# Kernel tuning notes

Hardware: AMD Instinct MI355X
Metric: run time of the kernel (lower is better)

## Reference

```python
import jax, jax.numpy as jnp
import numpy as np

S, D, P, R, E, M, K = 1024, 1024, 2816, 64, 8, 16, 1


def setup_inputs() -> dict:
    key = jax.random.key(0)
    ks = jax.random.split(key, 10)
    xav_a = (2.0 / (P + R)) ** 0.5   # xavier_uniform-like std for adapters
    xav_d = (2.0 / (D + P)) ** 0.5   # xavier for down projections
    bank_s = (1.0 / D) ** 0.5        # keep basis columns O(1)
    return {
        "hidden_states": jax.random.normal(ks[0], (S, D), jnp.float32),
        "expert_indices": jax.random.randint(ks[1], (S, K), 0, E),
        "expert_weights": jax.random.uniform(ks[2], (S, K), jnp.float32),
        "up_adapters": jax.random.normal(ks[3], (E, P, R), jnp.float32) * xav_a,
        "gate_adapters": jax.random.normal(ks[4], (E, P, R), jnp.float32) * xav_a,
        "up_mixture_logits": jax.random.normal(ks[5], (E, M), jnp.float32) * 0.01,
        "gate_mixture_logits": jax.random.normal(ks[6], (E, M), jnp.float32) * 0.01,
        "down_projections": jax.random.normal(ks[7], (E, D, P), jnp.float32) * xav_d,
        "up_bank": jax.random.normal(ks[8], (M, D, R), jnp.float32) * bank_s,
        "gate_bank": jax.random.normal(ks[9], (M, D, R), jnp.float32) * bank_s,
    }


def reference(hidden_states, expert_indices, expert_weights,
              up_adapters, gate_adapters, up_mixture_logits,
              gate_mixture_logits, down_projections, up_bank, gate_bank):
    n_experts = down_projections.shape[0]
    # SparseMixer: token-independent mixture weights over global bases (softmax)
    alpha_up = jax.nn.softmax(up_mixture_logits, axis=-1)      # [E, M]
    alpha_gate = jax.nn.softmax(gate_mixture_logits, axis=-1)  # [E, M]
    # Compose per-expert mixed bases: sum_j alpha_{e,j} B_j -> [E, D, R]
    up_mixed = jnp.einsum('em,mdr->edr', alpha_up, up_bank)
    gate_mixed = jnp.einsum('em,mdr->edr', alpha_gate, gate_bank)
    # Recomposed Up/Gate weights: A_e @ mixed_e^T -> [E, P, D]
    W_up = jnp.einsum('epr,edr->epd', up_adapters, up_mixed)
    W_gate = jnp.einsum('epr,edr->epd', gate_adapters, gate_mixed)
    # Combine routing weights per (token, expert): sum over topk slots
    onehot = (expert_indices[..., None] == jnp.arange(n_experts)).astype(hidden_states.dtype)  # [S,K,E]
    comb = jnp.einsum('ske,sk->se', onehot, expert_weights)  # [S, E]
    out = jnp.zeros_like(hidden_states)
    for e in range(n_experts):  # fixed small expert count
        up = hidden_states @ W_up[e].T        # [S, P]
        gate = hidden_states @ W_gate[e].T    # [S, P]
        inter = jax.nn.silu(gate) * up        # gated activation
        out = out + (inter @ down_projections[e].T) * comb[:, e:e + 1]
    return out
```

## Files before the change

kernel.cpp:

```cpp
#include <hip/hip_runtime.h>
#include <hip/hip_bf16.h>
#include <math.h>

#define S 1024
#define D 1024
#define P 2816
#define R 64
#define E 8
#define M 16
#define DSPLIT 4
#define KSPLIT 2
#define KHALF (P / KSPLIT)

typedef __attribute__((ext_vector_type(8))) short short8;
typedef __attribute__((ext_vector_type(4))) float floatx4;

static __device__ inline unsigned short f2bf(float f) {
  __hip_bfloat16 h = __float2bfloat16(f);
  return *reinterpret_cast<unsigned short*>(&h);
}

__global__ __launch_bounds__(256) void k_zero(float* __restrict__ out) {
  int i = blockIdx.x * 256 + threadIdx.x;
  *(float4*)(out + (size_t)i * 4) = make_float4(0.f, 0.f, 0.f, 0.f);
}

__global__ __launch_bounds__(256) void k_mix(
    const float* __restrict__ up_logits, const float* __restrict__ gate_logits,
    const float* __restrict__ up_bank, const float* __restrict__ gate_bank,
    unsigned short* __restrict__ mxu, unsigned short* __restrict__ mxg) {
  __shared__ float alpha[2][E][M];
  int t = threadIdx.x;
  if (t < 16) {
    int mat = t >> 3, e = t & 7;
    const float* lg = (mat ? gate_logits : up_logits) + e * M;
    float v[M], mx = -1e30f, s = 0.f;
#pragma unroll
    for (int m = 0; m < M; ++m) { v[m] = lg[m]; mx = fmaxf(mx, v[m]); }
#pragma unroll
    for (int m = 0; m < M; ++m) { v[m] = expf(v[m] - mx); s += v[m]; }
#pragma unroll
    for (int m = 0; m < M; ++m) alpha[mat][e][m] = v[m] / s;
  }
  __syncthreads();
  int g = blockIdx.x * 256 + t;
  int d = g >> 6, r = g & 63;
  float au[E] = {0, 0, 0, 0, 0, 0, 0, 0}, ag[E] = {0, 0, 0, 0, 0, 0, 0, 0};
#pragma unroll
  for (int m = 0; m < M; ++m) {
    float vu = up_bank[((size_t)m * D + d) * R + r];
    float vg = gate_bank[((size_t)m * D + d) * R + r];
#pragma unroll
    for (int e = 0; e < E; ++e) {
      au[e] += alpha[0][e][m] * vu;
      ag[e] += alpha[1][e][m] * vg;
    }
  }
#pragma unroll
  for (int e = 0; e < E; ++e) {
    mxu[((size_t)e * D + d) * R + r] = f2bf(au[e]);
    mxg[((size_t)e * D + d) * R + r] = f2bf(ag[e]);
  }
}

__global__ __launch_bounds__(1024) void k_sort(
    const int* __restrict__ idx, int* __restrict__ perm, int* __restrict__ offs) {
  __shared__ int hist[E];
  __shared__ int base[E];
  int t = threadIdx.x;
  if (t < E) hist[t] = 0;
  __syncthreads();
  int e = idx[t];
  atomicAdd(&hist[e], 1);
  __syncthreads();
  if (t == 0) {
    int run = 0;
    for (int i = 0; i < E; ++i) { base[i] = run; offs[i] = run; run += hist[i]; }
    offs[E] = S;
  }
  __syncthreads();
  int pos = atomicAdd(&base[e], 1);
  perm[pos] = t;
}

__global__ __launch_bounds__(256) void k_t(
    const float* __restrict__ H, const unsigned short* __restrict__ mxu,
    const unsigned short* __restrict__ mxg, const int* __restrict__ perm,
    const int* __restrict__ offs, float* __restrict__ tpart) {
  int e = blockIdx.x;
  int start = offs[e] + blockIdx.y * 128;
  int end = offs[e + 1];
  if (start >= end) return;
  int z = blockIdx.z;
  __shared__ unsigned short As[128][72];
  __shared__ unsigned short Bs[128][72];
  int t = threadIdx.x;
  int lane = t & 63, w = t >> 6, quad = lane >> 4, l15 = lane & 15;
  floatx4 acc[2][8];
#pragma unroll
  for (int tt = 0; tt < 2; ++tt)
#pragma unroll
    for (int nt = 0; nt < 8; ++nt) acc[tt][nt] = (floatx4){0.f, 0.f, 0.f, 0.f};

  int row_cache[4];
#pragma unroll
  for (int j = 0; j < 4; ++j) {
    int c = t + j * 256;
    int arow = c >> 3;
    int pos = start + arow;
    row_cache[j] = (pos < end) ? perm[pos] : -1;
  }

  for (int it = 0; it < 4; ++it) {
    int k0 = z * 256 + it * 64;
#pragma unroll
    for (int j = 0; j < 4; ++j) {
      int c = t + j * 256;
      int arow = c >> 3, acol = (c & 7) * 8;
      short8 v = (short8){0, 0, 0, 0, 0, 0, 0, 0};
      if (row_cache[j] >= 0) {
        const float* src = H + (size_t)row_cache[j] * D + k0 + acol;
        float4 f0 = *(const float4*)src;
        float4 f1 = *(const float4*)(src + 4);
        v[0] = f2bf(f0.x); v[1] = f2bf(f0.y); v[2] = f2bf(f0.z); v[3] = f2bf(f0.w);
        v[4] = f2bf(f1.x); v[5] = f2bf(f1.y); v[6] = f2bf(f1.z); v[7] = f2bf(f1.w);
      }
      *(short8*)&As[arow][acol] = v;
    }
    {
      int dd = t >> 2, r0 = (t & 3) * 16;
      const unsigned short* su = mxu + ((size_t)e * D + k0 + dd) * R + r0;
      const unsigned short* sg = mxg + ((size_t)e * D + k0 + dd) * R + r0;
      short8 u0 = *(const short8*)su, u1 = *(const short8*)(su + 8);
      short8 g0 = *(const short8*)sg, g1 = *(const short8*)(sg + 8);
#pragma unroll
      for (int j = 0; j < 8; ++j) {
        Bs[r0 + j][dd] = u0[j];
        Bs[r0 + 8 + j][dd] = u1[j];
        Bs[64 + r0 + j][dd] = g0[j];
        Bs[64 + r0 + 8 + j][dd] = g1[j];
      }
    }
    __syncthreads();
#pragma unroll
    for (int ks = 0; ks < 2; ++ks) {
      int kc = ks * 32 + quad * 8;
      short8 a[2], b[8];
#pragma unroll
      for (int tt = 0; tt < 2; ++tt) a[tt] = *(const short8*)&As[w * 32 + tt * 16 + l15][kc];
#pragma unroll
      for (int nt = 0; nt < 8; ++nt) b[nt] = *(const short8*)&Bs[nt * 16 + l15][kc];
#pragma unroll
      for (int tt = 0; tt < 2; ++tt)
#pragma unroll
        for (int nt = 0; nt < 8; ++nt)
          acc[tt][nt] = __builtin_amdgcn_mfma_f32_16x16x32_bf16(a[tt], b[nt], acc[tt][nt], 0, 0, 0);
    }
    __syncthreads();
  }
#pragma unroll
  for (int tt = 0; tt < 2; ++tt)
#pragma unroll
    for (int reg = 0; reg < 4; ++reg) {
      int row = w * 32 + tt * 16 + quad * 4 + reg;
      int pos = start + row;
      if (pos < end) {
#pragma unroll
        for (int nt = 0; nt < 8; ++nt)
          tpart[((size_t)z * S + pos) * 128 + nt * 16 + l15] = acc[tt][nt][reg];
      }
    }
}

__global__ __launch_bounds__(256) void k_tred(
    const float* __restrict__ tpart, unsigned short* __restrict__ tbuf) {
  int i = blockIdx.x * 256 + threadIdx.x;
  float s = 0.f;
#pragma unroll
  for (int ds = 0; ds < DSPLIT; ++ds) s += tpart[(size_t)ds * S * 128 + i];
  tbuf[i] = f2bf(s);
}

__global__ __launch_bounds__(256) void k_inter(
    const unsigned short* __restrict__ tbuf, const float* __restrict__ Aup,
    const float* __restrict__ Agate, const int* __restrict__ offs,
    unsigned short* __restrict__ inter) {
  int e = blockIdx.x;
  int start = offs[e] + blockIdx.y * 64;
  int end = offs[e + 1];
  if (start >= end) return;
  int p0 = blockIdx.z * 128;
  __shared__ unsigned short Ts[64][136];
  __shared__ unsigned short Bu[128][72];
  __shared__ unsigned short Bg[128][72];
  int t = threadIdx.x;
  int lane = t & 63, w = t >> 6;
#pragma unroll
  for (int j = 0; j < 4; ++j) {
    int i = t + j * 256;
    int row = i >> 4, c8 = (i & 15) * 8;
    int pos = start + row;
    float4 v = (pos < end) ? *(const float4*)(tbuf + (size_t)pos * 128 + c8)
                           : make_float4(0.f, 0.f, 0.f, 0.f);
    *(float4*)&Ts[row][c8] = v;
  }
#pragma unroll
  for (int j = 0; j < 4; ++j) {
    int i = t + j * 256;
    int pr = i >> 3, c8 = (i & 7) * 8;
    const float* su = Aup + ((size_t)(e * P + p0 + pr) * R + c8);
    const float* sg = Agate + ((size_t)(e * P + p0 + pr) * R + c8);
    float4 u0 = *(const float4*)su, u1 = *(const float4*)(su + 4);
    float4 g0 = *(const float4*)sg, g1 = *(const float4*)(sg + 4);
    short8 uv, gv;
    uv[0] = f2bf(u0.x); uv[1] = f2bf(u0.y); uv[2] = f2bf(u0.z); uv[3] = f2bf(u0.w);
    uv[4] = f2bf(u1.x); uv[5] = f2bf(u1.y); uv[6] = f2bf(u1.z); uv[7] = f2bf(u1.w);
    gv[0] = f2bf(g0.x); gv[1] = f2bf(g0.y); gv[2] = f2bf(g0.z); gv[3] = f2bf(g0.w);
    gv[4] = f2bf(g1.x); gv[5] = f2bf(g1.y); gv[6] = f2bf(g1.z); gv[7] = f2bf(g1.w);
    *(short8*)&Bu[pr][c8] = uv;
    *(short8*)&Bg[pr][c8] = gv;
  }
  __syncthreads();
  int quad = lane >> 4, l15 = lane & 15;
  floatx4 au_acc[4][2], ag_acc[4][2];
#pragma unroll
  for (int tt = 0; tt < 4; ++tt)
#pragma unroll
    for (int pt = 0; pt < 2; ++pt) {
      au_acc[tt][pt] = (floatx4){0.f, 0.f, 0.f, 0.f};
      ag_acc[tt][pt] = (floatx4){0.f, 0.f, 0.f, 0.f};
    }
#pragma unroll
  for (int ks = 0; ks < 2; ++ks) {
    int kc = ks * 32 + quad * 8;
    short8 au[4], ag[4], bu[2], bg[2];
#pragma unroll
    for (int tt = 0; tt < 4; ++tt) {
      au[tt] = *(const short8*)&Ts[tt * 16 + l15][kc];
      ag[tt] = *(const short8*)&Ts[tt * 16 + l15][64 + kc];
    }
#pragma unroll
    for (int pt = 0; pt < 2; ++pt) {
      bu[pt] = *(const short8*)&Bu[w * 32 + pt * 16 + l15][kc];
      bg[pt] = *(const short8*)&Bg[w * 32 + pt * 16 + l15][kc];
    }
#pragma unroll
    for (int tt = 0; tt < 4; ++tt)
#pragma unroll
      for (int pt = 0; pt < 2; ++pt) {
        au_acc[tt][pt] = __builtin_amdgcn_mfma_f32_16x16x32_bf16(au[tt], bu[pt], au_acc[tt][pt], 0, 0, 0);
        ag_acc[tt][pt] = __builtin_amdgcn_mfma_f32_16x16x32_bf16(ag[tt], bg[pt], ag_acc[tt][pt], 0, 0, 0);
      }
  }
#pragma unroll
  for (int tt = 0; tt < 4; ++tt)
#pragma unroll
    for (int reg = 0; reg < 4; ++reg) {
      int row = tt * 16 + quad * 4 + reg;
      int pos = start + row;
      if (pos < end) {
#pragma unroll
        for (int pt = 0; pt < 2; ++pt) {
          float g = ag_acc[tt][pt][reg];
          float u = au_acc[tt][pt][reg];
          float val = u * (g / (1.f + __expf(-g)));
          inter[(size_t)pos * P + p0 + w * 32 + pt * 16 + l15] = f2bf(val);
        }
      }
    }
}

__global__ __launch_bounds__(256) void k_down(
    const unsigned short* __restrict__ inter, const float* __restrict__ Wd,
    const int* __restrict__ perm, const int* __restrict__ offs,
    const float* __restrict__ wts, float* __restrict__ out) {
  int e = blockIdx.x;
  int start = offs[e];
  int end = offs[e + 1];
  if (start >= end) return;
  int kz = blockIdx.y;
  int d0 = blockIdx.z * 32;
  __shared__ unsigned short As[256][72];
  __shared__ unsigned short Bs[32][72];
  int t = threadIdx.x;
  int lane = t & 63, w = t >> 6, quad = lane >> 4, l15 = lane & 15;
  int brow = t >> 3, bcol = (t & 7) * 8;
  const float* bsrc = Wd + ((size_t)(e * D + d0 + brow) * P + bcol + kz * KHALF);
  floatx4 acc[4][2];
#pragma unroll
  for (int tt = 0; tt < 4; ++tt)
#pragma unroll
    for (int dt = 0; dt < 2; ++dt) acc[tt][dt] = (floatx4){0.f, 0.f, 0.f, 0.f};

  for (int it = 0; it < KHALF / 64; ++it) {
    int k0 = kz * KHALF + it * 64;
    {
      float4 b0 = *(const float4*)(bsrc + it * 64);
      float4 b1 = *(const float4*)(bsrc + it * 64 + 4);
      short8 bv;
      bv[0] = f2bf(b0.x); bv[1] = f2bf(b0.y); bv[2] = f2bf(b0.z); bv[3] = f2bf(b0.w);
      bv[4] = f2bf(b1.x); bv[5] = f2bf(b1.y); bv[6] = f2bf(b1.z); bv[7] = f2bf(b1.w);
      *(short8*)&Bs[brow][bcol] = bv;
    }
#pragma unroll
    for (int j = 0; j < 8; ++j) {
      int c = t + j * 256;
      int arow = c >> 3, acol = (c & 7) * 8;
      int pos = start + arow;
      float4 v = (pos < end) ? *(const float4*)(inter + (size_t)pos * P + k0 + acol)
                             : make_float4(0.f, 0.f, 0.f, 0.f);
      *(float4*)&As[arow][acol] = v;
    }
    __syncthreads();
#pragma unroll
    for (int ks = 0; ks < 2; ++ks) {
      int kc = ks * 32 + quad * 8;
      short8 a[4], b[2];
#pragma unroll
      for (int tt = 0; tt < 4; ++tt) a[tt] = *(const short8*)&As[w * 64 + tt * 16 + l15][kc];
#pragma unroll
      for (int dt = 0; dt < 2; ++dt) b[dt] = *(const short8*)&Bs[dt * 16 + l15][kc];
#pragma unroll
      for (int tt = 0; tt < 4; ++tt)
#pragma unroll
        for (int dt = 0; dt < 2; ++dt)
          acc[tt][dt] = __builtin_amdgcn_mfma_f32_16x16x32_bf16(a[tt], b[dt], acc[tt][dt], 0, 0, 0);
    }
    __syncthreads();
  }
#pragma unroll
  for (int tt = 0; tt < 4; ++tt)
#pragma unroll
    for (int reg = 0; reg < 4; ++reg) {
      int row = w * 64 + tt * 16 + quad * 4 + reg;
      int pos = start + row;
      if (pos < end) {
        int tok = perm[pos];
        float wt = wts[tok];
#pragma unroll
        for (int dt = 0; dt < 2; ++dt)
          atomicAdd(&out[(size_t)tok * D + d0 + dt * 16 + l15], acc[tt][dt][reg] * wt);
      }
    }
}

extern "C" void kernel_launch(void* const* d_in, const int* in_sizes, int n_in,
                              void* d_out, int out_size, void* d_ws, size_t ws_size,
                              hipStream_t stream) {
  const float* H = (const float*)d_in[0];
  const int* idx = (const int*)d_in[1];
  const float* wts = (const float*)d_in[2];
  const float* Aup = (const float*)d_in[3];
  const float* Agate = (const float*)d_in[4];
  const float* upl = (const float*)d_in[5];
  const float* gatel = (const float*)d_in[6];
  const float* Wd = (const float*)d_in[7];
  const float* upb = (const float*)d_in[8];
  const float* gateb = (const float*)d_in[9];
  float* out = (float*)d_out;

  char* ws = (char*)d_ws;
  unsigned short* mxu = (unsigned short*)ws;
  unsigned short* mxg = mxu + (size_t)E * D * R;
  float* tpart = (float*)(mxg + (size_t)E * D * R);
  unsigned short* tbuf = (unsigned short*)(tpart + (size_t)DSPLIT * S * 128);
  unsigned short* inter = tbuf + (size_t)S * 128;
  int* perm = (int*)(inter + (size_t)S * P);
  int* offs = perm + S;

  k_zero<<<S * D / 1024, 256, 0, stream>>>(out);
  k_mix<<<256, 256, 0, stream>>>(upl, gatel, upb, gateb, mxu, mxg);
  k_sort<<<1, 1024, 0, stream>>>(idx, perm, offs);
  k_t<<<dim3(E, 2, DSPLIT), 256, 0, stream>>>(H, mxu, mxg, perm, offs, tpart);
  k_tred<<<512, 256, 0, stream>>>(tpart, tbuf);
  k_inter<<<dim3(E, 4, P / 128), 256, 0, stream>>>(tbuf, Aup, Agate, offs, inter);
  k_down<<<dim3(E, KSPLIT, D / 32), 256, 0, stream>>>(inter, Wd, perm, offs, wts, out);
}
```

Baseline: 247.6 us.

## Fuse setup kernels, retile token GEMM, prefetch-pipeline down projection

Merges the output zeroing, the mixture-basis composition and the routing sort into one launch, dropping two kernel launches. The hidden-by-basis GEMM now uses 64-row tiles and splits the D reduction eight ways, giving more blocks and fewer accumulators per thread. The down-projection kernel widens its output tile to 64 columns and splits K four ways. It also prefetches the next K-step of inter and Wd into registers while the MFMAs run on the current shared-memory tile, hiding global-load latency. The trade-off is more partial-sum traffic in the reduce step, more registers held in k_down, and a serial sort running inside block 0 of the fused kernel.

```diff
diff --git a/kernel.cpp b/kernel.cpp
--- a/kernel.cpp
+++ b/kernel.cpp
@@ -8,9 +8,10 @@
 #define R 64
 #define E 8
 #define M 16
-#define DSPLIT 4
-#define KSPLIT 2
-#define KHALF (P / KSPLIT)
+#define DSPLIT 8
+#define KSPLIT 4
+#define KQ (P / KSPLIT)
+#define NIT (KQ / 64)
 
 typedef __attribute__((ext_vector_type(8))) short short8;
 typedef __attribute__((ext_vector_type(4))) float floatx4;
@@ -20,17 +21,44 @@
   return *reinterpret_cast<unsigned short*>(&h);
 }
 
-__global__ __launch_bounds__(256) void k_zero(float* __restrict__ out) {
-  int i = blockIdx.x * 256 + threadIdx.x;
-  *(float4*)(out + (size_t)i * 4) = make_float4(0.f, 0.f, 0.f, 0.f);
-}
-
-__global__ __launch_bounds__(256) void k_mix(
+__global__ __launch_bounds__(256) void k_pre(
     const float* __restrict__ up_logits, const float* __restrict__ gate_logits,
     const float* __restrict__ up_bank, const float* __restrict__ gate_bank,
-    unsigned short* __restrict__ mxu, unsigned short* __restrict__ mxg) {
+    const int* __restrict__ idx,
+    unsigned short* __restrict__ mxu, unsigned short* __restrict__ mxg,
+    int* __restrict__ perm, int* __restrict__ offs, float* __restrict__ out) {
+  int b = blockIdx.x, t = threadIdx.x;
+  float4 z4 = make_float4(0.f, 0.f, 0.f, 0.f);
+#pragma unroll
+  for (int j = 0; j < 4; ++j)
+    *(float4*)(out + (size_t)b * 4096 + j * 1024 + t * 4) = z4;
+
+  if (b == 0) {
+    __shared__ int hist[E];
+    __shared__ int basearr[E];
+    if (t < E) hist[t] = 0;
+    __syncthreads();
+    int e4[4];
+#pragma unroll
+    for (int j = 0; j < 4; ++j) {
+      e4[j] = idx[t + j * 256];
+      atomicAdd(&hist[e4[j]], 1);
+    }
+    __syncthreads();
+    if (t == 0) {
+      int run = 0;
+      for (int i = 0; i < E; ++i) { basearr[i] = run; offs[i] = run; run += hist[i]; }
+      offs[E] = S;
+    }
+    __syncthreads();
+#pragma unroll
+    for (int j = 0; j < 4; ++j) {
+      int pos = atomicAdd(&basearr[e4[j]], 1);
+      perm[pos] = t + j * 256;
+    }
+  }
+
   __shared__ float alpha[2][E][M];
-  int t = threadIdx.x;
   if (t < 16) {
     int mat = t >> 3, e = t & 7;
     const float* lg = (mat ? gate_logits : up_logits) + e * M;
@@ -43,7 +71,7 @@
     for (int m = 0; m < M; ++m) alpha[mat][e][m] = v[m] / s;
   }
   __syncthreads();
-  int g = blockIdx.x * 256 + t;
+  int g = b * 256 + t;
   int d = g >> 6, r = g & 63;
   float au[E] = {0, 0, 0, 0, 0, 0, 0, 0}, ag[E] = {0, 0, 0, 0, 0, 0, 0, 0};
 #pragma unroll
@@ -61,26 +89,6 @@
     mxu[((size_t)e * D + d) * R + r] = f2bf(au[e]);
     mxg[((size_t)e * D + d) * R + r] = f2bf(ag[e]);
   }
-}
-
-__global__ __launch_bounds__(1024) void k_sort(
-    const int* __restrict__ idx, int* __restrict__ perm, int* __restrict__ offs) {
-  __shared__ int hist[E];
-  __shared__ int base[E];
-  int t = threadIdx.x;
-  if (t < E) hist[t] = 0;
-  __syncthreads();
-  int e = idx[t];
-  atomicAdd(&hist[e], 1);
-  __syncthreads();
-  if (t == 0) {
-    int run = 0;
-    for (int i = 0; i < E; ++i) { base[i] = run; offs[i] = run; run += hist[i]; }
-    offs[E] = S;
-  }
-  __syncthreads();
-  int pos = atomicAdd(&base[e], 1);
-  perm[pos] = t;
 }
 
 __global__ __launch_bounds__(256) void k_t(
@@ -88,38 +96,34 @@
     const unsigned short* __restrict__ mxg, const int* __restrict__ perm,
     const int* __restrict__ offs, float* __restrict__ tpart) {
   int e = blockIdx.x;
-  int start = offs[e] + blockIdx.y * 128;
+  int start = offs[e] + blockIdx.y * 64;
   int end = offs[e + 1];
   if (start >= end) return;
   int z = blockIdx.z;
-  __shared__ unsigned short As[128][72];
+  __shared__ unsigned short As[64][72];
   __shared__ unsigned short Bs[128][72];
   int t = threadIdx.x;
   int lane = t & 63, w = t >> 6, quad = lane >> 4, l15 = lane & 15;
-  floatx4 acc[2][8];
-#pragma unroll
-  for (int tt = 0; tt < 2; ++tt)
-#pragma unroll
-    for (int nt = 0; nt < 8; ++nt) acc[tt][nt] = (floatx4){0.f, 0.f, 0.f, 0.f};
-
-  int row_cache[4];
-#pragma unroll
-  for (int j = 0; j < 4; ++j) {
+  int rows[2];
+#pragma unroll
+  for (int j = 0; j < 2; ++j) {
     int c = t + j * 256;
-    int arow = c >> 3;
-    int pos = start + arow;
-    row_cache[j] = (pos < end) ? perm[pos] : -1;
-  }
-
-  for (int it = 0; it < 4; ++it) {
-    int k0 = z * 256 + it * 64;
-#pragma unroll
-    for (int j = 0; j < 4; ++j) {
+    int pos = start + (c >> 3);
+    rows[j] = (pos < end) ? perm[pos] : -1;
+  }
+  floatx4 acc[8];
+#pragma unroll
+  for (int nt = 0; nt < 8; ++nt) acc[nt] = (floatx4){0.f, 0.f, 0.f, 0.f};
+
+  for (int it = 0; it < 2; ++it) {
+    int k0 = z * 128 + it * 64;
+#pragma unroll
+    for (int j = 0; j < 2; ++j) {
       int c = t + j * 256;
       int arow = c >> 3, acol = (c & 7) * 8;
       short8 v = (short8){0, 0, 0, 0, 0, 0, 0, 0};
-      if (row_cache[j] >= 0) {
-        const float* src = H + (size_t)row_cache[j] * D + k0 + acol;
+      if (rows[j] >= 0) {
+        const float* src = H + (size_t)rows[j] * D + k0 + acol;
         float4 f0 = *(const float4*)src;
         float4 f1 = *(const float4*)(src + 4);
         v[0] = f2bf(f0.x); v[1] = f2bf(f0.y); v[2] = f2bf(f0.z); v[3] = f2bf(f0.w);
@@ -145,31 +149,24 @@
 #pragma unroll
     for (int ks = 0; ks < 2; ++ks) {
       int kc = ks * 32 + quad * 8;
-      short8 a[2], b[8];
-#pragma unroll
-      for (int tt = 0; tt < 2; ++tt) a[tt] = *(const short8*)&As[w * 32 + tt * 16 + l15][kc];
-#pragma unroll
-      for (int nt = 0; nt < 8; ++nt) b[nt] = *(const short8*)&Bs[nt * 16 + l15][kc];
-#pragma unroll
-      for (int tt = 0; tt < 2; ++tt)
-#pragma unroll
-        for (int nt = 0; nt < 8; ++nt)
-          acc[tt][nt] = __builtin_amdgcn_mfma_f32_16x16x32_bf16(a[tt], b[nt], acc[tt][nt], 0, 0, 0);
-    }
-    __syncthreads();
-  }
-#pragma unroll
-  for (int tt = 0; tt < 2; ++tt)
-#pragma unroll
-    for (int reg = 0; reg < 4; ++reg) {
-      int row = w * 32 + tt * 16 + quad * 4 + reg;
-      int pos = start + row;
-      if (pos < end) {
-#pragma unroll
-        for (int nt = 0; nt < 8; ++nt)
-          tpart[((size_t)z * S + pos) * 128 + nt * 16 + l15] = acc[tt][nt][reg];
-      }
-    }
+      short8 a = *(const short8*)&As[w * 16 + l15][kc];
+#pragma unroll
+      for (int nt = 0; nt < 8; ++nt) {
+        short8 bb = *(const short8*)&Bs[nt * 16 + l15][kc];
+        acc[nt] = __builtin_amdgcn_mfma_f32_16x16x32_bf16(a, bb, acc[nt], 0, 0, 0);
+      }
+    }
+    __syncthreads();
+  }
+#pragma unroll
+  for (int reg = 0; reg < 4; ++reg) {
+    int pos = start + w * 16 + quad * 4 + reg;
+    if (pos < end) {
+#pragma unroll
+      for (int nt = 0; nt < 8; ++nt)
+        tpart[((size_t)z * S + pos) * 128 + nt * 16 + l15] = acc[nt][reg];
+    }
+  }
 }
 
 __global__ __launch_bounds__(256) void k_tred(
@@ -279,51 +276,71 @@
   int end = offs[e + 1];
   if (start >= end) return;
   int kz = blockIdx.y;
-  int d0 = blockIdx.z * 32;
+  int d0 = blockIdx.z * 64;
   __shared__ unsigned short As[256][72];
-  __shared__ unsigned short Bs[32][72];
+  __shared__ unsigned short Bs[64][72];
   int t = threadIdx.x;
   int lane = t & 63, w = t >> 6, quad = lane >> 4, l15 = lane & 15;
-  int brow = t >> 3, bcol = (t & 7) * 8;
-  const float* bsrc = Wd + ((size_t)(e * D + d0 + brow) * P + bcol + kz * KHALF);
-  floatx4 acc[4][2];
+
+  const unsigned short* aptr[8];
+  bool aok[8];
+#pragma unroll
+  for (int j = 0; j < 8; ++j) {
+    int arow = (t >> 3) + 32 * j;
+    int pos = start + arow;
+    aok[j] = (pos < end);
+    aptr[j] = inter + (size_t)(aok[j] ? pos : start) * P + kz * KQ + (t & 7) * 8;
+  }
+  const float* bsrc = Wd + ((size_t)(e * D + d0 + (t >> 2)) * P + kz * KQ + (t & 3) * 16);
+
+  float4 pa[8];
+  float4 pb[4];
+#pragma unroll
+  for (int j = 0; j < 8; ++j)
+    pa[j] = aok[j] ? *(const float4*)(aptr[j]) : make_float4(0.f, 0.f, 0.f, 0.f);
+#pragma unroll
+  for (int q = 0; q < 4; ++q) pb[q] = *(const float4*)(bsrc + q * 4);
+
+  floatx4 acc[4][4];
 #pragma unroll
   for (int tt = 0; tt < 4; ++tt)
 #pragma unroll
-    for (int dt = 0; dt < 2; ++dt) acc[tt][dt] = (floatx4){0.f, 0.f, 0.f, 0.f};
-
-  for (int it = 0; it < KHALF / 64; ++it) {
-    int k0 = kz * KHALF + it * 64;
+    for (int dt = 0; dt < 4; ++dt) acc[tt][dt] = (floatx4){0.f, 0.f, 0.f, 0.f};
+
+  for (int it = 0; it < NIT; ++it) {
+#pragma unroll
+    for (int j = 0; j < 8; ++j)
+      *(float4*)&As[(t >> 3) + 32 * j][(t & 7) * 8] = pa[j];
     {
-      float4 b0 = *(const float4*)(bsrc + it * 64);
-      float4 b1 = *(const float4*)(bsrc + it * 64 + 4);
-      short8 bv;
-      bv[0] = f2bf(b0.x); bv[1] = f2bf(b0.y); bv[2] = f2bf(b0.z); bv[3] = f2bf(b0.w);
-      bv[4] = f2bf(b1.x); bv[5] = f2bf(b1.y); bv[6] = f2bf(b1.z); bv[7] = f2bf(b1.w);
-      *(short8*)&Bs[brow][bcol] = bv;
-    }
-#pragma unroll
-    for (int j = 0; j < 8; ++j) {
-      int c = t + j * 256;
-      int arow = c >> 3, acol = (c & 7) * 8;
-      int pos = start + arow;
-      float4 v = (pos < end) ? *(const float4*)(inter + (size_t)pos * P + k0 + acol)
-                             : make_float4(0.f, 0.f, 0.f, 0.f);
-      *(float4*)&As[arow][acol] = v;
-    }
-    __syncthreads();
+      short8 bv0, bv1;
+      bv0[0] = f2bf(pb[0].x); bv0[1] = f2bf(pb[0].y); bv0[2] = f2bf(pb[0].z); bv0[3] = f2bf(pb[0].w);
+      bv0[4] = f2bf(pb[1].x); bv0[5] = f2bf(pb[1].y); bv0[6] = f2bf(pb[1].z); bv0[7] = f2bf(pb[1].w);
+      bv1[0] = f2bf(pb[2].x); bv1[1] = f2bf(pb[2].y); bv1[2] = f2bf(pb[2].z); bv1[3] = f2bf(pb[2].w);
+      bv1[4] = f2bf(pb[3].x); bv1[5] = f2bf(pb[3].y); bv1[6] = f2bf(pb[3].z); bv1[7] = f2bf(pb[3].w);
+      *(short8*)&Bs[t >> 2][(t & 3) * 16] = bv0;
+      *(short8*)&Bs[t >> 2][(t & 3) * 16 + 8] = bv1;
+    }
+    __syncthreads();
+    if (it + 1 < NIT) {
+      int k0 = (it + 1) * 64;
+#pragma unroll
+      for (int j = 0; j < 8; ++j)
+        pa[j] = aok[j] ? *(const float4*)(aptr[j] + k0) : make_float4(0.f, 0.f, 0.f, 0.f);
+#pragma unroll
+      for (int q = 0; q < 4; ++q) pb[q] = *(const float4*)(bsrc + k0 + q * 4);
+    }
 #pragma unroll
     for (int ks = 0; ks < 2; ++ks) {
       int kc = ks * 32 + quad * 8;
-      short8 a[4], b[2];
+      short8 a[4], b[4];
 #pragma unroll
       for (int tt = 0; tt < 4; ++tt) a[tt] = *(const short8*)&As[w * 64 + tt * 16 + l15][kc];
 #pragma unroll
-      for (int dt = 0; dt < 2; ++dt) b[dt] = *(const short8*)&Bs[dt * 16 + l15][kc];
+      for (int dt = 0; dt < 4; ++dt) b[dt] = *(const short8*)&Bs[dt * 16 + l15][kc];
 #pragma unroll
       for (int tt = 0; tt < 4; ++tt)
 #pragma unroll
-        for (int dt = 0; dt < 2; ++dt)
+        for (int dt = 0; dt < 4; ++dt)
           acc[tt][dt] = __builtin_amdgcn_mfma_f32_16x16x32_bf16(a[tt], b[dt], acc[tt][dt], 0, 0, 0);
     }
     __syncthreads();
@@ -332,13 +349,12 @@
   for (int tt = 0; tt < 4; ++tt)
 #pragma unroll
     for (int reg = 0; reg < 4; ++reg) {
-      int row = w * 64 + tt * 16 + quad * 4 + reg;
-      int pos = start + row;
+      int pos = start + w * 64 + tt * 16 + quad * 4 + reg;
       if (pos < end) {
         int tok = perm[pos];
         float wt = wts[tok];
 #pragma unroll
-        for (int dt = 0; dt < 2; ++dt)
+        for (int dt = 0; dt < 4; ++dt)
           atomicAdd(&out[(size_t)tok * D + d0 + dt * 16 + l15], acc[tt][dt][reg] * wt);
       }
     }
@@ -368,11 +384,9 @@
   int* perm = (int*)(inter + (size_t)S * P);
   int* offs = perm + S;
 
-  k_zero<<<S * D / 1024, 256, 0, stream>>>(out);
-  k_mix<<<256, 256, 0, stream>>>(upl, gatel, upb, gateb, mxu, mxg);
-  k_sort<<<1, 1024, 0, stream>>>(idx, perm, offs);
-  k_t<<<dim3(E, 2, DSPLIT), 256, 0, stream>>>(H, mxu, mxg, perm, offs, tpart);
+  k_pre<<<256, 256, 0, stream>>>(upl, gatel, upb, gateb, idx, mxu, mxg, perm, offs, out);
+  k_t<<<dim3(E, 4, DSPLIT), 256, 0, stream>>>(H, mxu, mxg, perm, offs, tpart);
   k_tred<<<512, 256, 0, stream>>>(tpart, tbuf);
   k_inter<<<dim3(E, 4, P / 128), 256, 0, stream>>>(tbuf, Aup, Agate, offs, inter);
-  k_down<<<dim3(E, KSPLIT, D / 32), 256, 0, stream>>>(inter, Wd, perm, offs, wts, out);
-}
+  k_down<<<dim3(E, KSPLIT, D / 64), 256, 0, stream>>>(inter, Wd, perm, offs, wts, out);
+}
```

After: 212.3 us. 1.17x faster.
